# Kernel optimization log

Measured on AMD Instinct MI355X. Metric: run time of the kernel, lower is better.

The kernel has to match this reference:

```python
import jax, jax.numpy as jnp
import numpy as np
import math

HIDDEN = 1024
N_HEADS = 16
HEAD_DIM = HIDDEN // N_HEADS
N_BLOCKS = 16
BATCH = 2
SEQ = 4096


def setup_inputs() -> dict:
    key = jax.random.key(0)
    ks = jax.random.split(key, 8)
    attention_input = jax.random.normal(ks[0], (BATCH, SEQ, HIDDEN), dtype=jnp.float32)
    attention_mask = jnp.ones((BATCH, SEQ), dtype=jnp.float32)
    # permutation over the num_blocks*num_heads flattened (block, head) axis
    permutation = jax.random.permutation(ks[1], N_BLOCKS * N_HEADS)
    init = 0.02
    q_w = jax.random.normal(ks[2], (HIDDEN, N_HEADS, HEAD_DIM), dtype=jnp.float32) * init
    q_b = jax.random.normal(ks[3], (N_HEADS, HEAD_DIM), dtype=jnp.float32) * init
    k_w = jax.random.normal(ks[4], (HIDDEN, N_HEADS, HEAD_DIM), dtype=jnp.float32) * init
    k_b = jax.random.normal(ks[5], (N_HEADS, HEAD_DIM), dtype=jnp.float32) * init
    v_w = jax.random.normal(ks[6], (HIDDEN, N_HEADS, HEAD_DIM), dtype=jnp.float32) * init
    v_b = jax.random.normal(ks[7], (N_HEADS, HEAD_DIM), dtype=jnp.float32) * init
    return {"attention_input": attention_input, "attention_mask": attention_mask,
            "permutation": permutation, "q_w": q_w, "q_b": q_b,
            "k_w": k_w, "k_b": k_b, "v_w": v_w, "v_b": v_b}


def reference(attention_input, attention_mask, permutation, q_w, q_b, k_w, k_b, v_w, v_b):
    B = attention_mask.shape[0]
    S = attention_mask.shape[1]
    nb = N_BLOCKS
    nh, d = q_b.shape
    blk = S // nb
    # QKV projections: [B,S,H] x [H,N,D] -> [B,S,N,D]
    q = jnp.einsum('bsh,hnd->bsnd', attention_input, q_w) + q_b
    k = jnp.einsum('bsh,hnd->bsnd', attention_input, k_w) + k_b
    v = jnp.einsum('bsh,hnd->bsnd', attention_input, v_w) + v_b

    def blockify(x):  # [B,S,N,D] -> [B, nb, nh, blk, d]
        return x.reshape(B, nb, blk, nh, d).transpose(0, 1, 3, 2, 4)

    q = blockify(q)
    # flatten (block, head) axis and gather per permutation
    k = blockify(k).reshape(B, nb * nh, blk, d)[:, permutation].reshape(B, nb, nh, blk, d)
    v = blockify(v).reshape(B, nb * nh, blk, d)[:, permutation].reshape(B, nb, nh, blk, d)

    scale = 1.0 / math.sqrt(float(d))
    logits = jnp.einsum('bgnqd,bgnkd->bgnqk', q, k) * scale  # block-local scores
    attn = jax.nn.softmax(logits, axis=-1)  # dropout prob 0 / eval mode
    ctx = jnp.einsum('bgnqk,bgnkd->bgnqd', attn, v)
    # [B,nb,nh,blk,d] -> [B,nb,blk,nh,d] -> [B,S,nh,d]
    return ctx.transpose(0, 1, 3, 2, 4).reshape(B, S, nh, d)
```

## Files before the change

kernel.cpp:

```cpp
#include <hip/hip_runtime.h>
#include <hip/hip_bf16.h>
#include <stdint.h>

typedef __attribute__((ext_vector_type(4))) float f32x4;
typedef __attribute__((ext_vector_type(8))) short s16x8;

__device__ inline short f2bf(float f) {
  union { float f; uint32_t u; } v; v.f = f;
  uint32_t r = v.u + 0x7fffu + ((v.u >> 16) & 1u);
  return (short)(r >> 16);
}

__device__ inline void gload_lds16(const void* g, void* l) {
  __builtin_amdgcn_global_load_lds((const __attribute__((address_space(1))) void*)g,
                                   (__attribute__((address_space(3))) void*)l,
                                   16, 0, 0);
}

#define MFMA16 __builtin_amdgcn_mfma_f32_16x16x32_bf16

__global__ __launch_bounds__(256) void k_prep(const float* __restrict__ x,
                                              short* __restrict__ xb,
                                              const float* __restrict__ qw,
                                              const float* __restrict__ kw,
                                              const float* __restrict__ vw,
                                              short* __restrict__ wt) {
  __shared__ float tile[64][65];
  int bx = blockIdx.x;
  if (bx < 4096) {
    int i = (bx * 256 + threadIdx.x) * 8;
    const float4* p = (const float4*)(x + i);
    float4 a = p[0], b = p[1];
    s16x8 o;
    o[0] = f2bf(a.x); o[1] = f2bf(a.y); o[2] = f2bf(a.z); o[3] = f2bf(a.w);
    o[4] = f2bf(b.x); o[5] = f2bf(b.y); o[6] = f2bf(b.z); o[7] = f2bf(b.w);
    *(s16x8*)(xb + i) = o;
    return;
  }
  bx -= 4096;
  int a  = bx >> 8;
  int t2 = bx & 255;
  int k0 = (t2 >> 4) << 6;
  int n0 = (t2 & 15) << 6;
  const float* w = (a == 0) ? qw : (a == 1) ? kw : vw;
  int c = threadIdx.x & 63, rr = threadIdx.x >> 6;
#pragma unroll
  for (int i = 0; i < 16; ++i) {
    int r = i * 4 + rr;
    tile[r][c] = w[(k0 + r) * 1024 + n0 + c];
  }
  __syncthreads();
  short* o = wt + a * 1048576;
#pragma unroll
  for (int i = 0; i < 16; ++i) {
    int r = i * 4 + rr;
    o[(n0 + r) * 1024 + k0 + c] = f2bf(tile[c][r]);
  }
}

__global__ __launch_bounds__(256, 2) void k_gemm(const short* __restrict__ xb,
                                                 const short* __restrict__ wt,
                                                 const float* __restrict__ qbias,
                                                 const float* __restrict__ kbias,
                                                 const float* __restrict__ vbias,
                                                 short* __restrict__ Qo,
                                                 short* __restrict__ Ko,
                                                 short* __restrict__ Vo) {
  __shared__ short lds[36864];
  const int tid = threadIdx.x, lane = tid & 63, wv = tid >> 6;
  const int wm = wv >> 1, wn = wv & 1;
  const int mt = blockIdx.x, by = blockIdx.y;
  const int a = by >> 3;
  const short* asrc = xb + (size_t)(mt * 256) * 1024;
  const short* bsrc = wt + (size_t)a * 1048576 + (size_t)((by & 7) * 128) * 1024;

  int srcA[4], dstA[4], srcB[2], dstB[2];
#pragma unroll
  for (int i = 0; i < 4; ++i) {
    int L = i * 256 + tid, s = L & 31;
    int row = (L >> 5) * 8 + (s >> 2);
    int c = (s & 3) ^ ((s >> 3) & 3);
    srcA[i] = row * 1024 + c * 8;
    dstA[i] = L * 16;
  }
#pragma unroll
  for (int i = 0; i < 2; ++i) {
    int L = i * 256 + tid, s = L & 31;
    int row = (L >> 5) * 8 + (s >> 2);
    int c = (s & 3) ^ ((s >> 3) & 3);
    srcB[i] = row * 1024 + c * 8;
    dstB[i] = 16384 + L * 16;
  }

  int aoff[8], boff[4];
#pragma unroll
  for (int m = 0; m < 8; ++m) {
    int row = wm * 128 + m * 16 + (lane & 15);
    aoff[m] = ((row >> 3) * 32 + (row & 7) * 4 + ((lane >> 4) ^ ((row >> 1) & 3))) * 16;
  }
#pragma unroll
  for (int n = 0; n < 4; ++n) {
    int row = wn * 64 + n * 16 + (lane & 15);
    boff[n] = 16384 + ((row >> 3) * 32 + (row & 7) * 4 + ((lane >> 4) ^ ((row >> 1) & 3))) * 16;
  }

  f32x4 acc[8][4] = {};

  auto STAGE = [&](int t, int bb) {
    const short* at = asrc + t * 32;
    const short* bt = bsrc + t * 32;
    char* l = (char*)lds + bb;
#pragma unroll
    for (int i = 0; i < 4; ++i) gload_lds16(at + srcA[i], l + dstA[i]);
#pragma unroll
    for (int i = 0; i < 2; ++i) gload_lds16(bt + srcB[i], l + dstB[i]);
  };

  STAGE(0, 0);
  STAGE(1, 24576);
  int bcur = 0, bpre = 49152;

  for (int t = 0; t < 31; ++t) {
    asm volatile("s_waitcnt vmcnt(6)" ::: "memory");
    __builtin_amdgcn_s_barrier();
    asm volatile("" ::: "memory");
    if (t < 30) STAGE(t + 2, bpre);
    const char* bufc = (const char*)lds + bcur;
    s16x8 af[8], bf[4];
#pragma unroll
    for (int m = 0; m < 8; ++m) af[m] = *(const s16x8*)(bufc + aoff[m]);
#pragma unroll
    for (int n = 0; n < 4; ++n) bf[n] = *(const s16x8*)(bufc + boff[n]);
    __builtin_amdgcn_s_setprio(1);
#pragma unroll
    for (int m = 0; m < 8; ++m)
#pragma unroll
      for (int n = 0; n < 4; ++n)
        acc[m][n] = MFMA16(af[m], bf[n], acc[m][n], 0, 0, 0);
    __builtin_amdgcn_s_setprio(0);
    bcur += 24576; if (bcur == 73728) bcur = 0;
    bpre += 24576; if (bpre == 73728) bpre = 0;
  }
  asm volatile("s_waitcnt vmcnt(0)" ::: "memory");
  __builtin_amdgcn_s_barrier();
  asm volatile("" ::: "memory");
  {
    const char* bufc = (const char*)lds + bcur;
    s16x8 af[8], bf[4];
#pragma unroll
    for (int m = 0; m < 8; ++m) af[m] = *(const s16x8*)(bufc + aoff[m]);
#pragma unroll
    for (int n = 0; n < 4; ++n) bf[n] = *(const s16x8*)(bufc + boff[n]);
    __builtin_amdgcn_s_setprio(1);
#pragma unroll
    for (int m = 0; m < 8; ++m)
#pragma unroll
      for (int n = 0; n < 4; ++n)
        acc[m][n] = MFMA16(af[m], bf[n], acc[m][n], 0, 0, 0);
    __builtin_amdgcn_s_setprio(0);
  }

  const float* bias = (a == 0) ? qbias : (a == 1) ? kbias : vbias;
  short* outp = (a == 0) ? Qo : (a == 1) ? Ko : Vo;
  int nbase = (by & 7) * 128 + wn * 64;
  int mbase = mt * 256 + wm * 128;
#pragma unroll
  for (int n = 0; n < 4; ++n) {
    int nloc = nbase + n * 16 + (lane & 15);
    float bv = bias[nloc];
    int head = nloc >> 6, d = nloc & 63;
#pragma unroll
    for (int m = 0; m < 8; ++m)
#pragma unroll
      for (int r = 0; r < 4; ++r) {
        int mm = mbase + m * 16 + ((lane >> 4) << 2) + r;
        outp[((size_t)head * 8192 + mm) * 64 + d] = f2bf(acc[m][n][r] + bv);
      }
  }
}

__global__ __launch_bounds__(256, 2) void k_attn(const short* __restrict__ Qb,
                                                 const short* __restrict__ Kb,
                                                 const short* __restrict__ Vb,
                                                 const int* __restrict__ perm,
                                                 float* __restrict__ out) {
  __shared__ short Ks[256 * 64];
  __shared__ short Vs[64 * 256];
  __shared__ short Ps[4 * 1024];

  int tid = threadIdx.x;
  int lane = tid & 63, wv = tid >> 6;
  int bx = blockIdx.x;
  int wg = (bx & 7) * 128 + (bx >> 3);
  int b = wg >> 9, g = (wg >> 5) & 15, n = (wg >> 1) & 15, h = wg & 1;
  int p = perm[g * 16 + n];
  int pg = p >> 4, ph = p & 15;

  const short* qsrc = Qb + ((size_t)n * 8192 + b * 4096 + g * 256 + h * 128) * 64;
  const short* ksrc = Kb + ((size_t)ph * 8192 + b * 4096 + pg * 256) * 64;
  const short* vsrc = Vb + ((size_t)ph * 8192 + b * 4096 + pg * 256) * 64;

  int qr0 = wv * 32;

#pragma unroll
  for (int i = 0; i < 8; ++i) {
    int c = i * 256 + tid;
    int row = c >> 3;
    int sc = ((c & 7) << 4) ^ ((row & 7) << 4);
    gload_lds16(ksrc + row * 64 + (sc >> 1), (char*)Ks + c * 16);
  }
  __builtin_amdgcn_sched_barrier(0);
  s16x8 vreg[8];
#pragma unroll
  for (int i = 0; i < 8; ++i) {
    int c = i * 256 + tid;
    int t = c >> 3;
    int d0 = (c & 7) << 3;
    vreg[i] = *(const s16x8*)(vsrc + t * 64 + d0);
  }
  s16x8 qreg[2][2];
#pragma unroll
  for (int rf = 0; rf < 2; ++rf)
#pragma unroll
    for (int ks = 0; ks < 2; ++ks) {
      int row = qr0 + rf * 16 + (lane & 15);
      qreg[rf][ks] = *(const s16x8*)(qsrc + row * 64 + ks * 32 + ((lane >> 4) << 3));
    }
  __builtin_amdgcn_sched_barrier(0);
  asm volatile("s_waitcnt vmcnt(12)" ::: "memory");
  __builtin_amdgcn_s_barrier();
  __builtin_amdgcn_sched_barrier(0);

  f32x4 accS[2][16] = {};
#pragma unroll
  for (int ks = 0; ks < 2; ++ks) {
    int cb = (ks << 6) + ((lane >> 4) << 4);
#pragma unroll
    for (int cf = 0; cf < 16; ++cf) {
      int row = cf * 16 + (lane & 15);
      s16x8 bk = *(const s16x8*)((const char*)Ks + row * 128 + (cb ^ ((row & 7) << 4)));
      accS[0][cf] = MFMA16(qreg[0][ks], bk, accS[0][cf], 0, 0, 0);
      accS[1][cf] = MFMA16(qreg[1][ks], bk, accS[1][cf], 0, 0, 0);
    }
  }

#pragma unroll
  for (int i = 0; i < 8; ++i) {
    int c = i * 256 + tid;
    int t = c >> 3;
    int d0 = (c & 7) << 3;
#pragma unroll
    for (int j = 0; j < 8; ++j) {
      int d = d0 + j;
      int sl = (d & 7) ^ ((d >> 3) & 7);
      int by = d * 512 + ((t * 2) ^ (sl << 4));
      *(short*)((char*)Vs + by) = vreg[i][j];
    }
  }
  __syncthreads();

  const float sc_log2e = 0.125f * 1.44269504088896f;
  float mx[2][4], inv[2][4];
#pragma unroll
  for (int rf = 0; rf < 2; ++rf)
#pragma unroll
    for (int r = 0; r < 4; ++r) {
      float m_ = accS[rf][0][r];
#pragma unroll
      for (int cf = 1; cf < 16; ++cf) m_ = fmaxf(m_, accS[rf][cf][r]);
#pragma unroll
      for (int msk = 1; msk < 16; msk <<= 1) m_ = fmaxf(m_, __shfl_xor(m_, msk));
      mx[rf][r] = m_;
    }
#pragma unroll
  for (int rf = 0; rf < 2; ++rf)
#pragma unroll
    for (int r = 0; r < 4; ++r) {
      float s_ = 0.f;
#pragma unroll
      for (int cf = 0; cf < 16; ++cf) {
        float e = exp2f((accS[rf][cf][r] - mx[rf][r]) * sc_log2e);
        accS[rf][cf][r] = e;
        s_ += e;
      }
#pragma unroll
      for (int msk = 1; msk < 16; msk <<= 1) s_ += __shfl_xor(s_, msk);
      inv[rf][r] = 1.0f / s_;
    }

  f32x4 accO[2][4] = {};
  short* pchunk = Ps + wv * 1024;
#pragma unroll
  for (int ks = 0; ks < 8; ++ks) {
#pragma unroll
    for (int rf = 0; rf < 2; ++rf)
#pragma unroll
      for (int half = 0; half < 2; ++half) {
        int cf = ks * 2 + half;
        int kvl = half * 16 + (lane & 15);
        int qp = (lane >> 4) << 2;
        int base = rf * 512 + ((kvl >> 3) << 7) + (kvl & 7);
#pragma unroll
        for (int r = 0; r < 4; ++r)
          pchunk[base + (qp + r) * 8] = f2bf(accS[rf][cf][r]);
      }
    int cbv = (ks << 6) + ((lane >> 4) << 4);
#pragma unroll
    for (int rf = 0; rf < 2; ++rf) {
      s16x8 ap = *(const s16x8*)(pchunk + rf * 512 + lane * 8);
#pragma unroll
      for (int dc = 0; dc < 4; ++dc) {
        int vrow = dc * 16 + (lane & 15);
        int sl = (vrow & 7) ^ ((vrow >> 3) & 7);
        s16x8 bv = *(const s16x8*)((const char*)Vs + vrow * 512 + (cbv ^ (sl << 4)));
        accO[rf][dc] = MFMA16(ap, bv, accO[rf][dc], 0, 0, 0);
      }
    }
  }

#pragma unroll
  for (int rf = 0; rf < 2; ++rf)
#pragma unroll
    for (int dc = 0; dc < 4; ++dc)
#pragma unroll
      for (int r = 0; r < 4; ++r) {
        int q = h * 128 + qr0 + rf * 16 + ((lane >> 4) << 2) + r;
        int d = dc * 16 + (lane & 15);
        out[(size_t)((b * 4096 + g * 256 + q) * 16 + n) * 64 + d] = accO[rf][dc][r] * inv[rf][r];
      }
}

extern "C" void kernel_launch(void* const* d_in, const int* in_sizes, int n_in,
                              void* d_out, int out_size, void* d_ws, size_t ws_size,
                              hipStream_t stream) {
  const float* x    = (const float*)d_in[0];
  const int*   perm = (const int*)d_in[2];
  const float* qw   = (const float*)d_in[3];
  const float* qb   = (const float*)d_in[4];
  const float* kw   = (const float*)d_in[5];
  const float* kb   = (const float*)d_in[6];
  const float* vw   = (const float*)d_in[7];
  const float* vb   = (const float*)d_in[8];
  float* out = (float*)d_out;

  char* ws = (char*)d_ws;
  short* Xb = (short*)(ws);
  short* Wt = (short*)(ws + 16777216UL);
  short* Qb = (short*)(ws + 23068672UL);
  short* Kb = (short*)(ws + 39845888UL);
  short* Vb = (short*)(ws + 56623104UL);

  k_prep<<<4864, 256, 0, stream>>>(x, Xb, qw, kw, vw, Wt);
  k_gemm<<<dim3(32, 24), 256, 0, stream>>>(Xb, Wt, qb, kb, vb, Qb, Kb, Vb);
  k_attn<<<1024, 256, 0, stream>>>(Qb, Kb, Vb, perm, out);
}
```

Measured before the change: 100.3 us.

## Process two block-heads per attention workgroup with 512 threads and prefetch

The attention kernel now runs 512 threads per workgroup, so each workgroup covers a full 256-query block, and it processes two (block, head) items in sequence. K and V for the second item are staged into LDS while the first item computes. V is now loaded directly to LDS via global_load_lds and transposed from there instead of going through registers. The aim is to hide global-load latency and cut launch and workgroup overhead. The cost is a large LDS footprint (about 144KB), which likely limits occupancy to one workgroup per CU, and a grid of only 256 workgroups.

```diff
diff --git a/kernel.cpp b/kernel.cpp
--- a/kernel.cpp
+++ b/kernel.cpp
@@ -179,155 +179,191 @@
   }
 }
 
-__global__ __launch_bounds__(256, 2) void k_attn(const short* __restrict__ Qb,
+__global__ __launch_bounds__(512, 2) void k_attn(const short* __restrict__ Qb,
                                                  const short* __restrict__ Kb,
                                                  const short* __restrict__ Vb,
                                                  const int* __restrict__ perm,
                                                  float* __restrict__ out) {
-  __shared__ short Ks[256 * 64];
-  __shared__ short Vs[64 * 256];
-  __shared__ short Ps[4 * 1024];
-
-  int tid = threadIdx.x;
-  int lane = tid & 63, wv = tid >> 6;
-  int bx = blockIdx.x;
-  int wg = (bx & 7) * 128 + (bx >> 3);
-  int b = wg >> 9, g = (wg >> 5) & 15, n = (wg >> 1) & 15, h = wg & 1;
-  int p = perm[g * 16 + n];
-  int pg = p >> 4, ph = p & 15;
-
-  const short* qsrc = Qb + ((size_t)n * 8192 + b * 4096 + g * 256 + h * 128) * 64;
-  const short* ksrc = Kb + ((size_t)ph * 8192 + b * 4096 + pg * 256) * 64;
-  const short* vsrc = Vb + ((size_t)ph * 8192 + b * 4096 + pg * 256) * 64;
-
-  int qr0 = wv * 32;
-
-#pragma unroll
-  for (int i = 0; i < 8; ++i) {
-    int c = i * 256 + tid;
-    int row = c >> 3;
-    int sc = ((c & 7) << 4) ^ ((row & 7) << 4);
-    gload_lds16(ksrc + row * 64 + (sc >> 1), (char*)Ks + c * 16);
-  }
-  __builtin_amdgcn_sched_barrier(0);
-  s16x8 vreg[8];
-#pragma unroll
-  for (int i = 0; i < 8; ++i) {
-    int c = i * 256 + tid;
-    int t = c >> 3;
-    int d0 = (c & 7) << 3;
-    vreg[i] = *(const s16x8*)(vsrc + t * 64 + d0);
-  }
-  s16x8 qreg[2][2];
-#pragma unroll
-  for (int rf = 0; rf < 2; ++rf)
-#pragma unroll
-    for (int ks = 0; ks < 2; ++ks) {
-      int row = qr0 + rf * 16 + (lane & 15);
-      qreg[rf][ks] = *(const s16x8*)(qsrc + row * 64 + ks * 32 + ((lane >> 4) << 3));
-    }
-  __builtin_amdgcn_sched_barrier(0);
-  asm volatile("s_waitcnt vmcnt(12)" ::: "memory");
+  __shared__ short lds[73728];
+  char* const L = (char*)lds;
+  const int tid = threadIdx.x;
+  const int lane = tid & 63, wv = tid >> 6;
+  const int qr0 = wv * 32;
+  const int wi0 = blockIdx.x * 2;
+
+  int bs[2], gs[2], ns[2];
+  const short* qsrcs[2];
+  const short* ksrcs[2];
+  const short* vsrcs[2];
+#pragma unroll
+  for (int it = 0; it < 2; ++it) {
+    int wi = wi0 + it;
+    int b = wi >> 8, g = (wi >> 4) & 15, n = wi & 15;
+    bs[it] = b; gs[it] = g; ns[it] = n;
+    int p = perm[g * 16 + n];
+    int pg = p >> 4, ph = p & 15;
+    qsrcs[it] = Qb + ((size_t)n * 8192 + b * 4096 + g * 256) * 64;
+    ksrcs[it] = Kb + ((size_t)ph * 8192 + b * 4096 + pg * 256) * 64;
+    vsrcs[it] = Vb + ((size_t)ph * 8192 + b * 4096 + pg * 256) * 64;
+  }
+
+  auto STAGE_K = [&](const short* ksrc, int off) {
+#pragma unroll
+    for (int i = 0; i < 4; ++i) {
+      int c = i * 512 + tid;
+      int row = c >> 3;
+      int sc = ((c & 7) << 4) ^ ((row & 7) << 4);
+      gload_lds16(ksrc + row * 64 + (sc >> 1), L + off + c * 16);
+    }
+  };
+  auto STAGE_V = [&](const short* vsrc) {
+#pragma unroll
+    for (int i = 0; i < 4; ++i) {
+      int c = i * 512 + tid;
+      int row = c >> 3;
+      int sc = ((c & 7) << 4) ^ ((row & 7) << 4);
+      gload_lds16(vsrc + row * 64 + (sc >> 1), L + 65536 + c * 16);
+    }
+  };
+  s16x8 qr[2][2][2];
+  auto LOAD_Q = [&](const short* qsrc, s16x8 (&dst)[2][2]) {
+#pragma unroll
+    for (int rf = 0; rf < 2; ++rf)
+#pragma unroll
+      for (int ks = 0; ks < 2; ++ks) {
+        int row = qr0 + rf * 16 + (lane & 15);
+        dst[rf][ks] = *(const s16x8*)(qsrc + row * 64 + ks * 32 + ((lane >> 4) << 3));
+      }
+  };
+
+  STAGE_K(ksrcs[0], 0);
+  STAGE_V(vsrcs[0]);
+  LOAD_Q(qsrcs[0], qr[0]);
+  asm volatile("s_waitcnt vmcnt(0)" ::: "memory");
   __builtin_amdgcn_s_barrier();
   __builtin_amdgcn_sched_barrier(0);
 
-  f32x4 accS[2][16] = {};
-#pragma unroll
-  for (int ks = 0; ks < 2; ++ks) {
-    int cb = (ks << 6) + ((lane >> 4) << 4);
-#pragma unroll
-    for (int cf = 0; cf < 16; ++cf) {
-      int row = cf * 16 + (lane & 15);
-      s16x8 bk = *(const s16x8*)((const char*)Ks + row * 128 + (cb ^ ((row & 7) << 4)));
-      accS[0][cf] = MFMA16(qreg[0][ks], bk, accS[0][cf], 0, 0, 0);
-      accS[1][cf] = MFMA16(qreg[1][ks], bk, accS[1][cf], 0, 0, 0);
-    }
-  }
-
-#pragma unroll
-  for (int i = 0; i < 8; ++i) {
-    int c = i * 256 + tid;
-    int t = c >> 3;
-    int d0 = (c & 7) << 3;
-#pragma unroll
-    for (int j = 0; j < 8; ++j) {
-      int d = d0 + j;
-      int sl = (d & 7) ^ ((d >> 3) & 7);
-      int by = d * 512 + ((t * 2) ^ (sl << 4));
-      *(short*)((char*)Vs + by) = vreg[i][j];
-    }
-  }
-  __syncthreads();
-
   const float sc_log2e = 0.125f * 1.44269504088896f;
-  float mx[2][4], inv[2][4];
-#pragma unroll
-  for (int rf = 0; rf < 2; ++rf)
-#pragma unroll
-    for (int r = 0; r < 4; ++r) {
-      float m_ = accS[rf][0][r];
-#pragma unroll
-      for (int cf = 1; cf < 16; ++cf) m_ = fmaxf(m_, accS[rf][cf][r]);
-#pragma unroll
-      for (int msk = 1; msk < 16; msk <<= 1) m_ = fmaxf(m_, __shfl_xor(m_, msk));
-      mx[rf][r] = m_;
-    }
-#pragma unroll
-  for (int rf = 0; rf < 2; ++rf)
-#pragma unroll
-    for (int r = 0; r < 4; ++r) {
-      float s_ = 0.f;
+
+#pragma unroll
+  for (int it = 0; it < 2; ++it) {
+    const char* ksb = L + it * 32768;
+    if (it == 0) {
+      STAGE_K(ksrcs[1], 32768);
+      __builtin_amdgcn_sched_barrier(0);
+    }
+
+    f32x4 accS[2][16] = {};
+#pragma unroll
+    for (int ks = 0; ks < 2; ++ks) {
+      int cb = (ks << 6) + ((lane >> 4) << 4);
 #pragma unroll
       for (int cf = 0; cf < 16; ++cf) {
-        float e = exp2f((accS[rf][cf][r] - mx[rf][r]) * sc_log2e);
-        accS[rf][cf][r] = e;
-        s_ += e;
-      }
-#pragma unroll
-      for (int msk = 1; msk < 16; msk <<= 1) s_ += __shfl_xor(s_, msk);
-      inv[rf][r] = 1.0f / s_;
-    }
-
-  f32x4 accO[2][4] = {};
-  short* pchunk = Ps + wv * 1024;
-#pragma unroll
-  for (int ks = 0; ks < 8; ++ks) {
+        int row = cf * 16 + (lane & 15);
+        s16x8 bk = *(const s16x8*)(ksb + row * 128 + (cb ^ ((row & 7) << 4)));
+        accS[0][cf] = MFMA16(qr[it][0][ks], bk, accS[0][cf], 0, 0, 0);
+        accS[1][cf] = MFMA16(qr[it][1][ks], bk, accS[1][cf], 0, 0, 0);
+      }
+    }
+
+#pragma unroll
+    for (int i = 0; i < 4; ++i) {
+      int c = i * 512 + tid;
+      int t = c >> 3;
+      int d0 = (c & 7) << 3;
+      s16x8 vv = *(const s16x8*)(L + 65536 + t * 128 + (((c & 7) << 4) ^ ((t & 7) << 4)));
+#pragma unroll
+      for (int j = 0; j < 8; ++j) {
+        int d = d0 + j;
+        int sl = (d & 7) ^ ((d >> 3) & 7);
+        *(short*)(L + 98304 + d * 512 + ((t * 2) ^ (sl << 4))) = vv[j];
+      }
+    }
+    asm volatile("s_waitcnt lgkmcnt(0)" ::: "memory");
+    __builtin_amdgcn_s_barrier();
+    __builtin_amdgcn_sched_barrier(0);
+    if (it == 0) {
+      STAGE_V(vsrcs[1]);
+      LOAD_Q(qsrcs[1], qr[1]);
+      __builtin_amdgcn_sched_barrier(0);
+    }
+
+    float mx[2][4], inv[2][4];
 #pragma unroll
     for (int rf = 0; rf < 2; ++rf)
 #pragma unroll
-      for (int half = 0; half < 2; ++half) {
-        int cf = ks * 2 + half;
-        int kvl = half * 16 + (lane & 15);
-        int qp = (lane >> 4) << 2;
-        int base = rf * 512 + ((kvl >> 3) << 7) + (kvl & 7);
-#pragma unroll
-        for (int r = 0; r < 4; ++r)
-          pchunk[base + (qp + r) * 8] = f2bf(accS[rf][cf][r]);
-      }
-    int cbv = (ks << 6) + ((lane >> 4) << 4);
-#pragma unroll
-    for (int rf = 0; rf < 2; ++rf) {
-      s16x8 ap = *(const s16x8*)(pchunk + rf * 512 + lane * 8);
-#pragma unroll
-      for (int dc = 0; dc < 4; ++dc) {
-        int vrow = dc * 16 + (lane & 15);
-        int sl = (vrow & 7) ^ ((vrow >> 3) & 7);
-        s16x8 bv = *(const s16x8*)((const char*)Vs + vrow * 512 + (cbv ^ (sl << 4)));
-        accO[rf][dc] = MFMA16(ap, bv, accO[rf][dc], 0, 0, 0);
-      }
-    }
-  }
-
-#pragma unroll
-  for (int rf = 0; rf < 2; ++rf)
-#pragma unroll
-    for (int dc = 0; dc < 4; ++dc)
-#pragma unroll
       for (int r = 0; r < 4; ++r) {
-        int q = h * 128 + qr0 + rf * 16 + ((lane >> 4) << 2) + r;
-        int d = dc * 16 + (lane & 15);
-        out[(size_t)((b * 4096 + g * 256 + q) * 16 + n) * 64 + d] = accO[rf][dc][r] * inv[rf][r];
-      }
+        float m_ = accS[rf][0][r];
+#pragma unroll
+        for (int cf = 1; cf < 16; ++cf) m_ = fmaxf(m_, accS[rf][cf][r]);
+#pragma unroll
+        for (int msk = 1; msk < 16; msk <<= 1) m_ = fmaxf(m_, __shfl_xor(m_, msk));
+        mx[rf][r] = m_;
+      }
+#pragma unroll
+    for (int rf = 0; rf < 2; ++rf)
+#pragma unroll
+      for (int r = 0; r < 4; ++r) {
+        float s_ = 0.f;
+#pragma unroll
+        for (int cf = 0; cf < 16; ++cf) {
+          float e = exp2f((accS[rf][cf][r] - mx[rf][r]) * sc_log2e);
+          accS[rf][cf][r] = e;
+          s_ += e;
+        }
+#pragma unroll
+        for (int msk = 1; msk < 16; msk <<= 1) s_ += __shfl_xor(s_, msk);
+        inv[rf][r] = 1.0f / s_;
+      }
+
+    f32x4 accO[2][4] = {};
+    short* pchunk = (short*)(L + 131072) + wv * 1024;
+#pragma unroll
+    for (int ks = 0; ks < 8; ++ks) {
+#pragma unroll
+      for (int rf = 0; rf < 2; ++rf)
+#pragma unroll
+        for (int half = 0; half < 2; ++half) {
+          int cf = ks * 2 + half;
+          int kvl = half * 16 + (lane & 15);
+          int qp = (lane >> 4) << 2;
+          int base = rf * 512 + ((kvl >> 3) << 7) + (kvl & 7);
+#pragma unroll
+          for (int r = 0; r < 4; ++r)
+            pchunk[base + (qp + r) * 8] = f2bf(accS[rf][cf][r]);
+        }
+      int cbv = (ks << 6) + ((lane >> 4) << 4);
+#pragma unroll
+      for (int rf = 0; rf < 2; ++rf) {
+        s16x8 ap = *(const s16x8*)(pchunk + rf * 512 + lane * 8);
+#pragma unroll
+        for (int dc = 0; dc < 4; ++dc) {
+          int vrow = dc * 16 + (lane & 15);
+          int sl = (vrow & 7) ^ ((vrow >> 3) & 7);
+          s16x8 bv = *(const s16x8*)(L + 98304 + vrow * 512 + (cbv ^ (sl << 4)));
+          accO[rf][dc] = MFMA16(ap, bv, accO[rf][dc], 0, 0, 0);
+        }
+      }
+    }
+
+    int b = bs[it], g = gs[it], n = ns[it];
+#pragma unroll
+    for (int rf = 0; rf < 2; ++rf)
+#pragma unroll
+      for (int dc = 0; dc < 4; ++dc)
+#pragma unroll
+        for (int r = 0; r < 4; ++r) {
+          int q = qr0 + rf * 16 + ((lane >> 4) << 2) + r;
+          int d = dc * 16 + (lane & 15);
+          out[(size_t)((b * 4096 + g * 256 + q) * 16 + n) * 64 + d] = accO[rf][dc][r] * inv[rf][r];
+        }
+
+    if (it == 0) {
+      asm volatile("s_waitcnt vmcnt(32) lgkmcnt(0)" ::: "memory");
+      __builtin_amdgcn_s_barrier();
+      __builtin_amdgcn_sched_barrier(0);
+    }
+  }
 }
 
 extern "C" void kernel_launch(void* const* d_in, const int* in_sizes, int n_in,
@@ -352,5 +388,5 @@
 
   k_prep<<<4864, 256, 0, stream>>>(x, Xb, qw, kw, vw, Wt);
   k_gemm<<<dim3(32, 24), 256, 0, stream>>>(Xb, Wt, qb, kb, vb, Qb, Kb, Vb);
-  k_attn<<<1024, 256, 0, stream>>>(Qb, Kb, Vb, perm, out);
-}
+  k_attn<<<256, 512, 0, stream>>>(Qb, Kb, Vb, perm, out);
+}
```

Result: slower. 109.5 us (+9.2%).

## Swizzle P staging layout, hoist V fragment loads, raise priority around MFMA

Applied to the files above, without the earlier changes.

Changes how the bf16 probability tile is written to and read from LDS: a lane-dependent XOR swizzle of row slots is meant to remove bank conflicts on the scalar short stores and the vector reads. The V B-operand fragments are now loaded once per k-step and reused for both row fragments instead of being reloaded inside the rf loop. s_setprio is raised around the QK^T and PV MFMA loops to favour matrix issue across waves. The result depends on the swizzle mapping exactly matching the MFMA A-operand layout, and the hoisted loads add register pressure.

```diff
diff --git a/kernel.cpp b/kernel.cpp
--- a/kernel.cpp
+++ b/kernel.cpp
@@ -232,6 +232,7 @@
   __builtin_amdgcn_sched_barrier(0);
 
   f32x4 accS[2][16] = {};
+  __builtin_amdgcn_s_setprio(1);
 #pragma unroll
   for (int ks = 0; ks < 2; ++ks) {
     int cb = (ks << 6) + ((lane >> 4) << 4);
@@ -243,6 +244,7 @@
       accS[1][cf] = MFMA16(qreg[1][ks], bk, accS[1][cf], 0, 0, 0);
     }
   }
+  __builtin_amdgcn_s_setprio(0);
 
 #pragma unroll
   for (int i = 0; i < 8; ++i) {
@@ -288,6 +290,16 @@
       inv[rf][r] = 1.0f / s_;
     }
 
+  const int g4 = lane >> 4;
+  const int s0l = (lane >> 3) & 1;
+  const int kv7 = lane & 7;
+  const int rs = ((lane & 1) ^ ((lane >> 3) & 1))
+               | ((((lane >> 1) & 1) ^ ((lane >> 4) & 1)) << 1)
+               | (((lane >> 2) & 1) << 2)
+               | (((lane >> 3) & 1) << 3)
+               | (((lane >> 4) & 1) << 4)
+               | (((lane >> 5) & 1) << 5);
+
   f32x4 accO[2][4] = {};
   short* pchunk = Ps + wv * 1024;
 #pragma unroll
@@ -297,25 +309,34 @@
 #pragma unroll
       for (int half = 0; half < 2; ++half) {
         int cf = ks * 2 + half;
-        int kvl = half * 16 + (lane & 15);
-        int qp = (lane >> 4) << 2;
-        int base = rf * 512 + ((kvl >> 3) << 7) + (kvl & 7);
-#pragma unroll
-        for (int r = 0; r < 4; ++r)
-          pchunk[base + (qp + r) * 8] = f2bf(accS[rf][cf][r]);
+#pragma unroll
+        for (int r = 0; r < 4; ++r) {
+          int slot = ((r & 1) ^ (g4 >> 1))
+                   | ((((r >> 1) & 1) ^ s0l) << 1)
+                   | ((g4 & 1) << 2)
+                   | ((g4 >> 1) << 3)
+                   | (s0l << 4)
+                   | (half << 5);
+          pchunk[rf * 512 + slot * 8 + kv7] = f2bf(accS[rf][cf][r]);
+        }
       }
     int cbv = (ks << 6) + ((lane >> 4) << 4);
+    s16x8 bv[4];
+#pragma unroll
+    for (int dc = 0; dc < 4; ++dc) {
+      int vrow = dc * 16 + (lane & 15);
+      int sl = (vrow & 7) ^ ((vrow >> 3) & 7);
+      bv[dc] = *(const s16x8*)((const char*)Vs + vrow * 512 + (cbv ^ (sl << 4)));
+    }
+    __builtin_amdgcn_s_setprio(1);
 #pragma unroll
     for (int rf = 0; rf < 2; ++rf) {
-      s16x8 ap = *(const s16x8*)(pchunk + rf * 512 + lane * 8);
-#pragma unroll
-      for (int dc = 0; dc < 4; ++dc) {
-        int vrow = dc * 16 + (lane & 15);
-        int sl = (vrow & 7) ^ ((vrow >> 3) & 7);
-        s16x8 bv = *(const s16x8*)((const char*)Vs + vrow * 512 + (cbv ^ (sl << 4)));
-        accO[rf][dc] = MFMA16(ap, bv, accO[rf][dc], 0, 0, 0);
-      }
-    }
+      s16x8 ap = *(const s16x8*)(pchunk + rf * 512 + rs * 8);
+#pragma unroll
+      for (int dc = 0; dc < 4; ++dc)
+        accO[rf][dc] = MFMA16(ap, bv[dc], accO[rf][dc], 0, 0, 0);
+    }
+    __builtin_amdgcn_s_setprio(0);
   }
 
 #pragma unroll
```

Result: no change. 100.4 us (+0.1%).
